# Kernel tuning notes

Measured on AMD Instinct MI355X. Metric: run time of the kernel, lower is better.

Reference implementation:

```python
import math
import jax, jax.numpy as jnp
import numpy as np

HEAD_DIM = 64

def setup_inputs() -> dict:
    key = jax.random.key(0)
    kq, kk, kv = jax.random.split(key, 3)
    B, S, D = 16, 2048, HEAD_DIM
    q = jax.random.normal(kq, (B, S, D), dtype=jnp.float32)
    k = jax.random.normal(kk, (B, S, D), dtype=jnp.float32)
    v = jax.random.normal(kv, (B, S, D), dtype=jnp.float32)
    return {"q": q, "k": k, "v": v}

def reference(q, k, v):
    # scores: [B, Sq, Sk]
    scores = jnp.einsum('bqd,bkd->bqk', q, k) / math.sqrt(HEAD_DIM)
    # NOTE: original uses nn.Softmax(dim=1) -> softmax over the QUERY axis
    weights = jax.nn.softmax(scores, axis=1)
    # dropout p=0.0 -> identity
    return jnp.einsum('bqk,bkd->bqd', weights, v)
```

## Files before the change

### kernel.cpp

```cpp
#include <hip/hip_runtime.h>
#include <hip/hip_bf16.h>

#define S_LEN 2048
#define D_DIM 64
#define NB 16

#define C_EXP 0.1803368801111204f

typedef __attribute__((ext_vector_type(8))) __bf16 bf16x8;
typedef __attribute__((ext_vector_type(4))) __bf16 bf16x4;
typedef __attribute__((ext_vector_type(4))) float f32x4;

#define GLOAD16(gp, lp)                                              \
  __builtin_amdgcn_global_load_lds(                                  \
      (const __attribute__((address_space(1))) void*)(gp),           \
      (__attribute__((address_space(3))) void*)(lp), 16, 0, 0)

__global__ __launch_bounds__(256) void convert_bf16_kernel(
    const float* __restrict__ qf, const float* __restrict__ kf,
    __bf16* __restrict__ qb, __bf16* __restrict__ kb) {
  const int n4 = NB * S_LEN * D_DIM / 4;
  for (int i = blockIdx.x * blockDim.x + threadIdx.x; i < n4;
       i += gridDim.x * blockDim.x) {
    float4 a = ((const float4*)qf)[i];
    float4 c = ((const float4*)kf)[i];
    bf16x4 oa = {(__bf16)a.x, (__bf16)a.y, (__bf16)a.z, (__bf16)a.w};
    bf16x4 oc = {(__bf16)c.x, (__bf16)c.y, (__bf16)c.z, (__bf16)c.w};
    ((bf16x4*)qb)[i] = oa;
    ((bf16x4*)kb)[i] = oc;
  }
}

__global__ __launch_bounds__(256) void stats_kernel(
    const __bf16* __restrict__ Qb, const __bf16* __restrict__ Kb,
    float* __restrict__ Lpart, int qlen) {
  __shared__ __align__(16) __bf16 QT[4096];
  const int b = blockIdx.y;
  const int kblk = blockIdx.x;
  const int qs = blockIdx.z;
  const int tid = threadIdx.x;
  const int wave = tid >> 6;
  const int lane = tid & 63;
  const int l16 = lane & 15;
  const int g = lane >> 4;

  const int kbase = kblk * 128 + wave * 32;
  bf16x8 ak[2][2];
#pragma unroll
  for (int rg = 0; rg < 2; ++rg) {
    const __bf16* kp =
        Kb + ((size_t)b * S_LEN + kbase + rg * 16 + l16) * D_DIM + g * 8;
    ak[rg][0] = *(const bf16x8*)(kp);
    ak[rg][1] = *(const bf16x8*)(kp + 32);
  }

  const int srow = tid >> 3;
  const int scol = 8 * ((tid & 7) ^ (srow & 7));

  float sacc[2][4] = {};
  const __bf16* Qbase = Qb + (size_t)b * S_LEN * D_DIM;
  const int qbeg = qs * qlen;

  for (int q0 = qbeg; q0 < qbeg + qlen; q0 += 64) {
    __syncthreads();
#pragma unroll
    for (int h = 0; h < 2; ++h)
      GLOAD16(Qbase + (size_t)(q0 + h * 32 + srow) * D_DIM + scol,
              (char*)QT + h * 4096 + (size_t)tid * 16);
    asm volatile("s_waitcnt vmcnt(0)" ::: "memory");
    __syncthreads();

#pragma unroll
    for (int qt = 0; qt < 4; ++qt) {
      const int r = qt * 16 + l16;
      bf16x8 bq0 = *(const bf16x8*)(QT + r * 64 + 8 * (g ^ (r & 7)));
      bf16x8 bq1 = *(const bf16x8*)(QT + r * 64 + 8 * ((g + 4) ^ (r & 7)));
#pragma unroll
      for (int rg = 0; rg < 2; ++rg) {
        f32x4 t = __builtin_amdgcn_mfma_f32_16x16x32_bf16(
            ak[rg][0], bq0, (f32x4){0.f, 0.f, 0.f, 0.f}, 0, 0, 0);
        t = __builtin_amdgcn_mfma_f32_16x16x32_bf16(ak[rg][1], bq1, t, 0, 0, 0);
#pragma unroll
        for (int r4 = 0; r4 < 4; ++r4)
          sacc[rg][r4] += __builtin_amdgcn_exp2f(t[r4] * C_EXP);
      }
    }
  }
#pragma unroll
  for (int rg = 0; rg < 2; ++rg)
#pragma unroll
    for (int r4 = 0; r4 < 4; ++r4) {
      float v = sacc[rg][r4];
      v += __shfl_xor(v, 1);
      v += __shfl_xor(v, 2);
      v += __shfl_xor(v, 4);
      v += __shfl_xor(v, 8);
      if (l16 == 0)
        Lpart[(size_t)qs * NB * S_LEN + (size_t)b * S_LEN + kbase + rg * 16 +
              g * 4 + r4] = v;
    }
}

__global__ __launch_bounds__(256) void scalev_kernel(
    const float* __restrict__ V, const float* __restrict__ Lpart,
    __bf16* __restrict__ Vt) {
  const int b = blockIdx.y;
  const int k = blockIdx.x * 256 + threadIdx.x;
  const size_t NS = (size_t)NB * S_LEN;
  const size_t idx = (size_t)b * S_LEN + k;
  const float L =
      Lpart[idx] + Lpart[NS + idx] + Lpart[2 * NS + idx] + Lpart[3 * NS + idx];
  const float inv = 1.0f / L;
  const float* vrow = V + ((size_t)b * S_LEN + k) * D_DIM;
  __bf16* vt = Vt + (size_t)b * D_DIM * S_LEN + k;
#pragma unroll
  for (int d = 0; d < D_DIM; ++d)
    vt[(size_t)d * S_LEN] = (__bf16)(vrow[d] * inv);
}

__global__ __launch_bounds__(256) void attn_out_kernel(
    const __bf16* __restrict__ Qb, const __bf16* __restrict__ Kb,
    const __bf16* __restrict__ Vt, float* __restrict__ Op, int klen) {
  __shared__ __align__(16) __bf16 KT[4096];
  __shared__ __align__(16) __bf16 VT[4096];
  __shared__ __align__(16) __bf16 Plds[4][32][72];
  const int b = blockIdx.y;
  const int qblk = blockIdx.x;
  const int ks = blockIdx.z;
  const int tid = threadIdx.x;
  const int wave = tid >> 6;
  const int lane = tid & 63;
  const int l16 = lane & 15;
  const int g = lane >> 4;

  const int qbase = qblk * 128 + wave * 32;
  bf16x8 aq[2][2];
#pragma unroll
  for (int rg = 0; rg < 2; ++rg) {
    const __bf16* qp =
        Qb + ((size_t)b * S_LEN + qbase + rg * 16 + l16) * D_DIM + g * 8;
    aq[rg][0] = *(const bf16x8*)(qp);
    aq[rg][1] = *(const bf16x8*)(qp + 32);
  }

  f32x4 acc[2][4] = {};
  const int srow = tid >> 3;
  const int scol = 8 * ((tid & 7) ^ (srow & 7));
  const __bf16* Kbase = Kb + (size_t)b * S_LEN * D_DIM;
  const __bf16* Vbase = Vt + (size_t)b * D_DIM * S_LEN;
  __bf16(*pl)[72] = Plds[wave];
  const int kbeg = ks * klen;

  for (int k0 = kbeg; k0 < kbeg + klen; k0 += 64) {
    __syncthreads();
#pragma unroll
    for (int h = 0; h < 2; ++h) {
      GLOAD16(Kbase + (size_t)(k0 + h * 32 + srow) * D_DIM + scol,
              (char*)KT + h * 4096 + (size_t)tid * 16);
      GLOAD16(Vbase + (size_t)(h * 32 + srow) * S_LEN + k0 + scol,
              (char*)VT + h * 4096 + (size_t)tid * 16);
    }
    asm volatile("s_waitcnt vmcnt(0)" ::: "memory");
    __syncthreads();

#pragma unroll
    for (int kt = 0; kt < 4; ++kt) {
      const int r = kt * 16 + l16;
      bf16x8 bk0 = *(const bf16x8*)(KT + r * 64 + 8 * (g ^ (r & 7)));
      bf16x8 bk1 = *(const bf16x8*)(KT + r * 64 + 8 * ((g + 4) ^ (r & 7)));
#pragma unroll
      for (int rg = 0; rg < 2; ++rg) {
        f32x4 t = __builtin_amdgcn_mfma_f32_16x16x32_bf16(
            aq[rg][0], bk0, (f32x4){0.f, 0.f, 0.f, 0.f}, 0, 0, 0);
        t = __builtin_amdgcn_mfma_f32_16x16x32_bf16(aq[rg][1], bk1, t, 0, 0, 0);
#pragma unroll
        for (int r4 = 0; r4 < 4; ++r4)
          pl[rg * 16 + g * 4 + r4][kt * 16 + l16] =
              (__bf16)__builtin_amdgcn_exp2f(t[r4] * C_EXP);
      }
    }
    bf16x8 pa[2][2];
#pragma unroll
    for (int rg = 0; rg < 2; ++rg) {
      pa[rg][0] = *(const bf16x8*)(&pl[rg * 16 + l16][g * 8]);
      pa[rg][1] = *(const bf16x8*)(&pl[rg * 16 + l16][32 + g * 8]);
    }
#pragma unroll
    for (int dt = 0; dt < 4; ++dt) {
      const int rd = dt * 16 + l16;
      bf16x8 bv0 = *(const bf16x8*)(VT + rd * 64 + 8 * (g ^ (rd & 7)));
      bf16x8 bv1 = *(const bf16x8*)(VT + rd * 64 + 8 * ((g + 4) ^ (rd & 7)));
#pragma unroll
      for (int rg = 0; rg < 2; ++rg) {
        acc[rg][dt] =
            __builtin_amdgcn_mfma_f32_16x16x32_bf16(pa[rg][0], bv0, acc[rg][dt], 0, 0, 0);
        acc[rg][dt] =
            __builtin_amdgcn_mfma_f32_16x16x32_bf16(pa[rg][1], bv1, acc[rg][dt], 0, 0, 0);
      }
    }
  }
  float* ob = Op + ((size_t)ks * NB + b) * (size_t)(S_LEN * D_DIM);
#pragma unroll
  for (int rg = 0; rg < 2; ++rg)
#pragma unroll
    for (int dt = 0; dt < 4; ++dt)
#pragma unroll
      for (int r4 = 0; r4 < 4; ++r4)
        ob[(size_t)(qbase + rg * 16 + g * 4 + r4) * D_DIM + dt * 16 + l16] =
            acc[rg][dt][r4];
}

__global__ __launch_bounds__(256) void reduce_kernel(
    const float* __restrict__ Op, float* __restrict__ out, int np) {
  const int i = blockIdx.x * 256 + threadIdx.x;
  const int slab = NB * S_LEN * D_DIM / 4;
  const float4* p = (const float4*)Op;
  float4 s = p[i];
  for (int j = 1; j < np; ++j) {
    float4 t = p[i + (size_t)j * slab];
    s.x += t.x; s.y += t.y; s.z += t.z; s.w += t.w;
  }
  ((float4*)out)[i] = s;
}

extern "C" void kernel_launch(void* const* d_in, const int* in_sizes, int n_in,
                              void* d_out, int out_size, void* d_ws,
                              size_t ws_size, hipStream_t stream) {
  const float* q = (const float*)d_in[0];
  const float* k = (const float*)d_in[1];
  const float* v = (const float*)d_in[2];
  float* out = (float*)d_out;

  char* ws = (char*)d_ws;
  const size_t nelem = (size_t)NB * S_LEN * D_DIM;
  __bf16* Qb = (__bf16*)ws;
  __bf16* Kb = (__bf16*)(ws + nelem * 2);
  __bf16* Vt = (__bf16*)(ws + nelem * 4);
  float* Lp = (float*)(ws + nelem * 6);
  float* Op = (float*)(ws + (13u << 20));

  int ksplit = 1;
  if (ws_size >= (13u << 20) + 4 * nelem * 4) ksplit = 4;
  else if (ws_size >= (13u << 20) + 2 * nelem * 4) ksplit = 2;

  convert_bf16_kernel<<<1024, 256, 0, stream>>>(q, k, Qb, Kb);
  stats_kernel<<<dim3(16, 16, 4), 256, 0, stream>>>(Qb, Kb, Lp, S_LEN / 4);
  scalev_kernel<<<dim3(8, 16), 256, 0, stream>>>(v, Lp, Vt);
  float* attn_dst = (ksplit == 1) ? out : Op;
  attn_out_kernel<<<dim3(16, 16, ksplit), 256, 0, stream>>>(Qb, Kb, Vt,
                                                            attn_dst,
                                                            S_LEN / ksplit);
  if (ksplit > 1)
    reduce_kernel<<<(int)(nelem / 4 / 256), 256, 0, stream>>>(Op, out, ksplit);
}
```

Measured before the change: 135.3 us.

## Prefetch next Q/K/V tiles into LDS to overlap loads with MFMA

```diff
diff --git a/kernel.cpp b/kernel.cpp
--- a/kernel.cpp
+++ b/kernel.cpp
@@ -15,6 +15,9 @@
   __builtin_amdgcn_global_load_lds(                                  \
       (const __attribute__((address_space(1))) void*)(gp),           \
       (__attribute__((address_space(3))) void*)(lp), 16, 0, 0)
+
+#define BAR() asm volatile("s_barrier" ::: "memory")
+#define WAIT_VM(n) asm volatile("s_waitcnt vmcnt(" #n ")" ::: "memory")
 
 __global__ __launch_bounds__(256) void convert_bf16_kernel(
     const float* __restrict__ qf, const float* __restrict__ kf,
@@ -34,7 +37,7 @@
 __global__ __launch_bounds__(256) void stats_kernel(
     const __bf16* __restrict__ Qb, const __bf16* __restrict__ Kb,
     float* __restrict__ Lpart, int qlen) {
-  __shared__ __align__(16) __bf16 QT[4096];
+  __shared__ __align__(16) __bf16 QT[2][4096];
   const int b = blockIdx.y;
   const int kblk = blockIdx.x;
   const int qs = blockIdx.z;
@@ -60,21 +63,32 @@
   float sacc[2][4] = {};
   const __bf16* Qbase = Qb + (size_t)b * S_LEN * D_DIM;
   const int qbeg = qs * qlen;
-
-  for (int q0 = qbeg; q0 < qbeg + qlen; q0 += 64) {
-    __syncthreads();
-#pragma unroll
-    for (int h = 0; h < 2; ++h)
-      GLOAD16(Qbase + (size_t)(q0 + h * 32 + srow) * D_DIM + scol,
-              (char*)QT + h * 4096 + (size_t)tid * 16);
-    asm volatile("s_waitcnt vmcnt(0)" ::: "memory");
-    __syncthreads();
-
-#pragma unroll
-    for (int qt = 0; qt < 4; ++qt) {
-      const int r = qt * 16 + l16;
-      bf16x8 bq0 = *(const bf16x8*)(QT + r * 64 + 8 * (g ^ (r & 7)));
-      bf16x8 bq1 = *(const bf16x8*)(QT + r * 64 + 8 * ((g + 4) ^ (r & 7)));
+  const int qend = qbeg + qlen;
+
+#pragma unroll
+  for (int h = 0; h < 2; ++h)
+    GLOAD16(Qbase + (size_t)(qbeg + h * 32 + srow) * D_DIM + scol,
+            (char*)QT[0] + h * 4096 + (size_t)tid * 16);
+
+  int cur = 0;
+  for (int q0 = qbeg; q0 < qend; q0 += 64, cur ^= 1) {
+    const bool haveNext = (q0 + 64 < qend);
+    if (haveNext) {
+#pragma unroll
+      for (int h = 0; h < 2; ++h)
+        GLOAD16(Qbase + (size_t)(q0 + 64 + h * 32 + srow) * D_DIM + scol,
+                (char*)QT[cur ^ 1] + h * 4096 + (size_t)tid * 16);
+      WAIT_VM(2);
+    } else {
+      WAIT_VM(0);
+    }
+    BAR();
+    const __bf16* qt = QT[cur];
+#pragma unroll
+    for (int qtl = 0; qtl < 4; ++qtl) {
+      const int r = qtl * 16 + l16;
+      bf16x8 bq0 = *(const bf16x8*)(qt + r * 64 + 8 * (g ^ (r & 7)));
+      bf16x8 bq1 = *(const bf16x8*)(qt + r * 64 + 8 * ((g + 4) ^ (r & 7)));
 #pragma unroll
       for (int rg = 0; rg < 2; ++rg) {
         f32x4 t = __builtin_amdgcn_mfma_f32_16x16x32_bf16(
@@ -85,6 +99,7 @@
           sacc[rg][r4] += __builtin_amdgcn_exp2f(t[r4] * C_EXP);
       }
     }
+    BAR();
   }
 #pragma unroll
   for (int rg = 0; rg < 2; ++rg)
@@ -150,19 +165,21 @@
   const __bf16* Vbase = Vt + (size_t)b * D_DIM * S_LEN;
   __bf16(*pl)[72] = Plds[wave];
   const int kbeg = ks * klen;
-
-  for (int k0 = kbeg; k0 < kbeg + klen; k0 += 64) {
-    __syncthreads();
-#pragma unroll
-    for (int h = 0; h < 2; ++h) {
-      GLOAD16(Kbase + (size_t)(k0 + h * 32 + srow) * D_DIM + scol,
-              (char*)KT + h * 4096 + (size_t)tid * 16);
-      GLOAD16(Vbase + (size_t)(h * 32 + srow) * S_LEN + k0 + scol,
-              (char*)VT + h * 4096 + (size_t)tid * 16);
-    }
-    asm volatile("s_waitcnt vmcnt(0)" ::: "memory");
-    __syncthreads();
-
+  const int kend = kbeg + klen;
+
+#pragma unroll
+  for (int h = 0; h < 2; ++h)
+    GLOAD16(Kbase + (size_t)(kbeg + h * 32 + srow) * D_DIM + scol,
+            (char*)KT + h * 4096 + (size_t)tid * 16);
+#pragma unroll
+  for (int h = 0; h < 2; ++h)
+    GLOAD16(Vbase + (size_t)(h * 32 + srow) * S_LEN + kbeg + scol,
+            (char*)VT + h * 4096 + (size_t)tid * 16);
+
+  for (int k0 = kbeg; k0 < kend; k0 += 64) {
+    const bool haveNext = (k0 + 64 < kend);
+    WAIT_VM(2);
+    BAR();
 #pragma unroll
     for (int kt = 0; kt < 4; ++kt) {
       const int r = kt * 16 + l16;
@@ -179,6 +196,17 @@
               (__bf16)__builtin_amdgcn_exp2f(t[r4] * C_EXP);
       }
     }
+    BAR();
+    if (haveNext) {
+#pragma unroll
+      for (int h = 0; h < 2; ++h)
+        GLOAD16(Kbase + (size_t)(k0 + 64 + h * 32 + srow) * D_DIM + scol,
+                (char*)KT + h * 4096 + (size_t)tid * 16);
+      WAIT_VM(2);
+    } else {
+      WAIT_VM(0);
+    }
+    BAR();
     bf16x8 pa[2][2];
 #pragma unroll
     for (int rg = 0; rg < 2; ++rg) {
@@ -192,11 +220,18 @@
       bf16x8 bv1 = *(const bf16x8*)(VT + rd * 64 + 8 * ((g + 4) ^ (rd & 7)));
 #pragma unroll
       for (int rg = 0; rg < 2; ++rg) {
-        acc[rg][dt] =
-            __builtin_amdgcn_mfma_f32_16x16x32_bf16(pa[rg][0], bv0, acc[rg][dt], 0, 0, 0);
-        acc[rg][dt] =
-            __builtin_amdgcn_mfma_f32_16x16x32_bf16(pa[rg][1], bv1, acc[rg][dt], 0, 0, 0);
+        acc[rg][dt] = __builtin_amdgcn_mfma_f32_16x16x32_bf16(
+            pa[rg][0], bv0, acc[rg][dt], 0, 0, 0);
+        acc[rg][dt] = __builtin_amdgcn_mfma_f32_16x16x32_bf16(
+            pa[rg][1], bv1, acc[rg][dt], 0, 0, 0);
       }
+    }
+    BAR();
+    if (haveNext) {
+#pragma unroll
+      for (int h = 0; h < 2; ++h)
+        GLOAD16(Vbase + (size_t)(h * 32 + srow) * S_LEN + (k0 + 64) + scol,
+                (char*)VT + h * 4096 + (size_t)tid * 16);
     }
   }
   float* ob = Op + ((size_t)ks * NB + b) * (size_t)(S_LEN * D_DIM);
```

New measurement: 131.1 us. 3.1% less time.
